# Kernel tuning notes

Measured on AMD Instinct MI355X. Metric: run time of the kernel, lower is better.

The kernel has to match this reference:

```python
import jax, jax.numpy as jnp
import numpy as np

B, T, C, NH = 8, 1024, 1024, 16
DH = C // NH  # 64


def setup_inputs() -> dict:
    key = jax.random.key(0)
    ks = jax.random.split(key, 7)
    s = 1.0 / np.sqrt(C)
    return {
        "x": jax.random.normal(ks[0], (B, T, C), dtype=jnp.float32),
        "Wq": jax.random.normal(ks[1], (C, C), dtype=jnp.float32) * s,
        "bq": jnp.zeros((C,), dtype=jnp.float32),
        "Wk": jax.random.normal(ks[2], (C, C), dtype=jnp.float32) * s,
        "bk": jnp.zeros((C,), dtype=jnp.float32),
        "Wv": jax.random.normal(ks[3], (C, C), dtype=jnp.float32) * s,
        "bv": jnp.zeros((C,), dtype=jnp.float32),
    }


def reference(x, Wq, bq, Wk, bk, Wv, bv):
    # Linear projections (weights stored as [in, out])
    q = x @ Wq + bq  # [B, T, C]
    k = x @ Wk + bk
    v = x @ Wv + bv
    q = q.reshape(B, T, NH, DH)
    k = k.reshape(B, T, NH, DH)
    v = v.reshape(B, T, NH, DH)
    scale = 1.0 / np.sqrt(DH)
    # NOTE: source module's causal mask buffer is all-ones due to a non-inplace
    # masked_fill bug, so attention is NON-causal (mask multiply is a no-op).
    attn = jnp.einsum("bqhd,bkhd->bhqk", q, k) * scale  # [B, NH, T, T]
    attn = jax.nn.softmax(attn, axis=-1)
    # dropout is identity (p=0 / eval)
    o = jnp.einsum("bhqk,bkhd->bqhd", attn, v)  # [B, T, NH, DH]
    return o.reshape(B, T, C)
```

## Files before the change

### kernel.cpp

```cpp
#include <hip/hip_runtime.h>


#define B_  8
#define T_  1024
#define C_  1024
#define NH_ 16
#define DH_ 64
#define M_  (B_ * T_)

typedef __bf16 bf16x8 __attribute__((ext_vector_type(8)));
typedef float  floatx4 __attribute__((ext_vector_type(4)));

__device__ __forceinline__ unsigned short f2bf(float f) {
    unsigned int u = __float_as_uint(f);
    unsigned int r = (u + 0x7fffu + ((u >> 16) & 1u)) >> 16;
    return (unsigned short)r;
}

__device__ __forceinline__ void gload_lds16(const void* g, void* l) {
    __builtin_amdgcn_global_load_lds(
        (const __attribute__((address_space(1))) unsigned int*)g,
        (__attribute__((address_space(3))) unsigned int*)l, 16, 0, 0);
}

__global__ __launch_bounds__(256) void cast_x_kernel(
    const float* __restrict__ x, unsigned short* __restrict__ xb, int n4)
{
    int i = blockIdx.x * 256 + threadIdx.x;
    if (i < n4) {
        float4 v = ((const float4*)x)[i];
        ushort4 o;
        o.x = f2bf(v.x); o.y = f2bf(v.y); o.z = f2bf(v.z); o.w = f2bf(v.w);
        ((ushort4*)xb)[i] = o;
    }
}

__global__ __launch_bounds__(256) void transpose_w_kernel(
    const float* __restrict__ Wq, const float* __restrict__ Wk,
    const float* __restrict__ Wv, unsigned short* __restrict__ WtAll)
{
    int which = blockIdx.y;
    const float* W = (which == 0) ? Wq : ((which == 1) ? Wk : Wv);
    unsigned short* out = WtAll + (size_t)which * C_ * C_;

    __shared__ __align__(16) unsigned short tile[64 * 65];
    int tb = blockIdx.x;
    int k0 = (tb >> 4) * 64, n0 = (tb & 15) * 64;
    int c = threadIdx.x & 63, r0 = threadIdx.x >> 6;

    for (int j = 0; j < 16; ++j) {
        int r = r0 + j * 4;
        tile[c * 65 + r] = f2bf(W[(size_t)(k0 + r) * C_ + n0 + c]);
    }
    __syncthreads();
    for (int j = 0; j < 16; ++j) {
        int r = r0 + j * 4;
        out[(size_t)(n0 + r) * C_ + k0 + c] = tile[r * 65 + c];
    }
}

__global__ __launch_bounds__(256) void qkv_gemm_kernel(
    const unsigned short* __restrict__ xb,
    const unsigned short* __restrict__ WtAll,
    const float* __restrict__ bq, const float* __restrict__ bk,
    const float* __restrict__ bv,
    unsigned short* __restrict__ Qb, unsigned short* __restrict__ Kb,
    unsigned short* __restrict__ Vb)
{
    int which = blockIdx.z;
    const unsigned short* W = WtAll + (size_t)which * C_ * C_;
    const float* bias = (which == 0) ? bq : ((which == 1) ? bk : bv);
    unsigned short* outp = (which == 0) ? Qb : ((which == 1) ? Kb : Vb);
    float oscale = (which == 0) ? 0.125f : 1.0f;

    __shared__ __align__(16) unsigned short As[128 * 64];
    __shared__ __align__(16) unsigned short Bs[128 * 64];

    int tid = threadIdx.x;
    int wave = tid >> 6, lane = tid & 63;
    int quad = lane >> 4, l16 = lane & 15, l7 = l16 & 7;
    int wm = wave >> 1, wn = wave & 1;
    int bm = blockIdx.x, bn = blockIdx.y;

    floatx4 acc[4][4] = {};

    for (int kk = 0; kk < C_; kk += 64) {
        __syncthreads();
        #pragma unroll
        for (int i = 0; i < 4; ++i) {
            int c = (wave * 4 + i) * 64 + lane;
            int row = c >> 3;
            int lcol = ((c & 7) ^ (row & 7)) * 8;
            gload_lds16(&xb[(size_t)(bm * 128 + row) * C_ + kk + lcol],
                        &As[(wave * 4 + i) * 512]);
            gload_lds16(&W[(size_t)(bn * 128 + row) * C_ + kk + lcol],
                        &Bs[(wave * 4 + i) * 512]);
        }
        __syncthreads();
        #pragma unroll
        for (int s = 0; s < 2; ++s) {
            bf16x8 a[4], bfr[4];
            #pragma unroll
            for (int mt = 0; mt < 4; ++mt) {
                int row = wm * 64 + mt * 16 + l16;
                a[mt] = *(const bf16x8*)&As[row * 64 + (((s * 4 + quad)) ^ l7) * 8];
            }
            #pragma unroll
            for (int nt = 0; nt < 4; ++nt) {
                int row = wn * 64 + nt * 16 + l16;
                bfr[nt] = *(const bf16x8*)&Bs[row * 64 + (((s * 4 + quad)) ^ l7) * 8];
            }
            #pragma unroll
            for (int mt = 0; mt < 4; ++mt)
                #pragma unroll
                for (int nt = 0; nt < 4; ++nt)
                    acc[mt][nt] = __builtin_amdgcn_mfma_f32_16x16x32_bf16(
                        a[mt], bfr[nt], acc[mt][nt], 0, 0, 0);
        }
    }

    #pragma unroll
    for (int nt = 0; nt < 4; ++nt) {
        int colg = bn * 128 + wn * 64 + nt * 16 + l16;
        int h = colg >> 6, d = colg & 63;
        float bval = bias[colg];
        #pragma unroll
        for (int mt = 0; mt < 4; ++mt) {
            #pragma unroll
            for (int reg = 0; reg < 4; ++reg) {
                int rowg = bm * 128 + wm * 64 + mt * 16 + quad * 4 + reg;
                int bb = rowg >> 10, t = rowg & (T_ - 1);
                float val = (acc[mt][nt][reg] + bval) * oscale;
                outp[((size_t)(bb * NH_ + h) * T_ + t) * DH_ + d] = f2bf(val);
            }
        }
    }
}

__global__ __launch_bounds__(256) void transpose_v_kernel(
    const unsigned short* __restrict__ Vb, unsigned short* __restrict__ Vt)
{
    int bh = blockIdx.y;
    int t0 = blockIdx.x * 64;
    const unsigned short* src = Vb + (size_t)bh * T_ * DH_;
    unsigned short* dst = Vt + (size_t)bh * DH_ * T_;
    __shared__ unsigned short tile[64 * 66];
    int c = threadIdx.x & 63, r0 = threadIdx.x >> 6;
    #pragma unroll
    for (int j = 0; j < 16; ++j) {
        int r = r0 * 16 + j;
        tile[r * 66 + c] = src[(size_t)(t0 + r) * DH_ + c];
    }
    __syncthreads();
    #pragma unroll
    for (int j = 0; j < 16; ++j) {
        int d = r0 * 16 + j;
        dst[(size_t)d * T_ + t0 + c] = tile[c * 66 + d];
    }
}

__global__ __launch_bounds__(256) void attn_kernel(
    const unsigned short* __restrict__ Qb,
    const unsigned short* __restrict__ Kb,
    const unsigned short* __restrict__ Vt,
    float* __restrict__ out)
{
    int bh = blockIdx.x;
    int qblk = blockIdx.y;
    int b = bh >> 4, h = bh & (NH_ - 1);
    int tid = threadIdx.x;
    int wave = tid >> 6, lane = tid & 63;
    int quad = lane >> 4, l16 = lane & 15, l7 = l16 & 7;

    const unsigned short* Qh = Qb + (size_t)bh * T_ * DH_;
    const unsigned short* Kh = Kb + (size_t)bh * T_ * DH_;
    const unsigned short* Vh = Vt + (size_t)bh * DH_ * T_;

    __shared__ __align__(16) unsigned short Ks[64 * 64];
    __shared__ __align__(16) unsigned short Vs[64 * 64];
    __shared__ __align__(16) unsigned short Ps[4][16 * 72];

    bf16x8 qa[2][2];
    #pragma unroll
    for (int mt = 0; mt < 2; ++mt) {
        int qrow = qblk * 128 + (wave * 2 + mt) * 16 + l16;
        qa[mt][0] = *(const bf16x8*)&Qh[(size_t)qrow * DH_ + quad * 8];
        qa[mt][1] = *(const bf16x8*)&Qh[(size_t)qrow * DH_ + 32 + quad * 8];
    }

    floatx4 o_acc[2][4] = {};
    float l_i[2][4] = {};

    for (int kt = 0; kt < T_ / 64; ++kt) {
        __syncthreads();
        #pragma unroll
        for (int i = 0; i < 2; ++i) {
            int c = (wave * 2 + i) * 64 + lane;
            int row = c >> 3;
            int lcol = ((c & 7) ^ (row & 7)) * 8;
            gload_lds16(&Kh[(size_t)(kt * 64 + row) * DH_ + lcol],
                        &Ks[(wave * 2 + i) * 512]);
            gload_lds16(&Vh[(size_t)row * T_ + kt * 64 + lcol],
                        &Vs[(wave * 2 + i) * 512]);
        }
        __syncthreads();

        bf16x8 kb[4][2];
        #pragma unroll
        for (int nt = 0; nt < 4; ++nt) {
            int r = (nt * 16 + l16) * 64;
            kb[nt][0] = *(const bf16x8*)&Ks[r + ((quad    ) ^ l7) * 8];
            kb[nt][1] = *(const bf16x8*)&Ks[r + ((quad + 4) ^ l7) * 8];
        }

        #pragma unroll
        for (int mt = 0; mt < 2; ++mt) {
            floatx4 s[4] = {};
            #pragma unroll
            for (int nt = 0; nt < 4; ++nt) {
                s[nt] = __builtin_amdgcn_mfma_f32_16x16x32_bf16(qa[mt][0], kb[nt][0], s[nt], 0, 0, 0);
                s[nt] = __builtin_amdgcn_mfma_f32_16x16x32_bf16(qa[mt][1], kb[nt][1], s[nt], 0, 0, 0);
            }
            #pragma unroll
            for (int reg = 0; reg < 4; ++reg) {
                float e0 = __expf(s[0][reg]), e1 = __expf(s[1][reg]);
                float e2 = __expf(s[2][reg]), e3 = __expf(s[3][reg]);
                s[0][reg] = e0; s[1][reg] = e1; s[2][reg] = e2; s[3][reg] = e3;
                float rs = (e0 + e1) + (e2 + e3);
                rs += __shfl_xor(rs, 1); rs += __shfl_xor(rs, 2);
                rs += __shfl_xor(rs, 4); rs += __shfl_xor(rs, 8);
                l_i[mt][reg] += rs;
            }
            #pragma unroll
            for (int nt = 0; nt < 4; ++nt)
                #pragma unroll
                for (int reg = 0; reg < 4; ++reg)
                    Ps[wave][(quad * 4 + reg) * 72 + nt * 16 + l16] = f2bf(s[nt][reg]);
            #pragma unroll
            for (int s2 = 0; s2 < 2; ++s2) {
                bf16x8 pa = *(const bf16x8*)&Ps[wave][l16 * 72 + s2 * 32 + quad * 8];
                #pragma unroll
                for (int nt = 0; nt < 4; ++nt) {
                    bf16x8 vb = *(const bf16x8*)&Vs[(nt * 16 + l16) * 64 + ((s2 * 4 + quad) ^ l7) * 8];
                    o_acc[mt][nt] = __builtin_amdgcn_mfma_f32_16x16x32_bf16(pa, vb, o_acc[mt][nt], 0, 0, 0);
                }
            }
        }
    }

    #pragma unroll
    for (int mt = 0; mt < 2; ++mt) {
        float inv[4];
        #pragma unroll
        for (int reg = 0; reg < 4; ++reg) inv[reg] = 1.0f / l_i[mt][reg];
        #pragma unroll
        for (int nt = 0; nt < 4; ++nt) {
            int d = nt * 16 + l16;
            #pragma unroll
            for (int reg = 0; reg < 4; ++reg) {
                int t = qblk * 128 + (wave * 2 + mt) * 16 + quad * 4 + reg;
                out[((size_t)b * T_ + t) * C_ + h * DH_ + d] = o_acc[mt][nt][reg] * inv[reg];
            }
        }
    }
}

extern "C" void kernel_launch(void* const* d_in, const int* in_sizes, int n_in,
                              void* d_out, int out_size, void* d_ws, size_t ws_size,
                              hipStream_t stream) {
    const float* x  = (const float*)d_in[0];
    const float* Wq = (const float*)d_in[1];
    const float* bq = (const float*)d_in[2];
    const float* Wk = (const float*)d_in[3];
    const float* bk = (const float*)d_in[4];
    const float* Wv = (const float*)d_in[5];
    const float* bv = (const float*)d_in[6];
    float* out = (float*)d_out;

    char* ws = (char*)d_ws;
    size_t off = 0;
    unsigned short* xb = (unsigned short*)(ws + off); off += (size_t)M_ * C_ * 2;
    unsigned short* Wt = (unsigned short*)(ws + off); off += (size_t)3 * C_ * C_ * 2;
    unsigned short* Qb = (unsigned short*)(ws + off); off += (size_t)M_ * C_ * 2;
    unsigned short* Kb = (unsigned short*)(ws + off); off += (size_t)M_ * C_ * 2;
    unsigned short* Vb = (unsigned short*)(ws + off); off += (size_t)M_ * C_ * 2;
    unsigned short* Vt = xb;

    int n4 = (M_ * C_) / 4;
    cast_x_kernel<<<dim3(n4 / 256), dim3(256), 0, stream>>>(x, xb, n4);

    transpose_w_kernel<<<dim3(256, 3), dim3(256), 0, stream>>>(Wq, Wk, Wv, Wt);

    qkv_gemm_kernel<<<dim3(M_ / 128, C_ / 128, 3), dim3(256), 0, stream>>>(
        xb, Wt, bq, bk, bv, Qb, Kb, Vb);

    transpose_v_kernel<<<dim3(T_ / 64, B_ * NH_), dim3(256), 0, stream>>>(Vb, Vt);

    attn_kernel<<<dim3(B_ * NH_, T_ / 128), dim3(256), 0, stream>>>(Qb, Kb, Vt, out);
}
```

Before: 250.7 us.

## Fuse V transpose into QKV epilogue and transpose attention MFMA operands

The QKV GEMM now writes V directly in transposed [bh, d, t] layout, which removes the separate transpose_v kernel launch and its extra read and write of V. The attention kernel swaps MFMA operand order so S^T and O^T are computed. That turns row sums into cross-quad shuffles, lets P be stored with vectorized ushort4 writes, and lets the output be stored as float4 rows. Softmax uses exp2f with log2e folded into the Q scale. The transposed V store in the GEMM epilogue is strided along t, so those writes are less coalesced.

```diff
diff --git a/kernel.cpp b/kernel.cpp
--- a/kernel.cpp
+++ b/kernel.cpp
@@ -65,13 +65,13 @@
     const float* __restrict__ bq, const float* __restrict__ bk,
     const float* __restrict__ bv,
     unsigned short* __restrict__ Qb, unsigned short* __restrict__ Kb,
-    unsigned short* __restrict__ Vb)
+    unsigned short* __restrict__ Vt)
 {
     int which = blockIdx.z;
     const unsigned short* W = WtAll + (size_t)which * C_ * C_;
     const float* bias = (which == 0) ? bq : ((which == 1) ? bk : bv);
-    unsigned short* outp = (which == 0) ? Qb : ((which == 1) ? Kb : Vb);
-    float oscale = (which == 0) ? 0.125f : 1.0f;
+    unsigned short* outp = (which == 0) ? Qb : ((which == 1) ? Kb : Vt);
+    float oscale = (which == 0) ? 0.125f * 1.44269504f : 1.0f;
 
     __shared__ __align__(16) unsigned short As[128 * 64];
     __shared__ __align__(16) unsigned short Bs[128 * 64];
@@ -131,31 +131,14 @@
                 int rowg = bm * 128 + wm * 64 + mt * 16 + quad * 4 + reg;
                 int bb = rowg >> 10, t = rowg & (T_ - 1);
                 float val = (acc[mt][nt][reg] + bval) * oscale;
-                outp[((size_t)(bb * NH_ + h) * T_ + t) * DH_ + d] = f2bf(val);
-            }
-        }
-    }
-}
-
-__global__ __launch_bounds__(256) void transpose_v_kernel(
-    const unsigned short* __restrict__ Vb, unsigned short* __restrict__ Vt)
-{
-    int bh = blockIdx.y;
-    int t0 = blockIdx.x * 64;
-    const unsigned short* src = Vb + (size_t)bh * T_ * DH_;
-    unsigned short* dst = Vt + (size_t)bh * DH_ * T_;
-    __shared__ unsigned short tile[64 * 66];
-    int c = threadIdx.x & 63, r0 = threadIdx.x >> 6;
-    #pragma unroll
-    for (int j = 0; j < 16; ++j) {
-        int r = r0 * 16 + j;
-        tile[r * 66 + c] = src[(size_t)(t0 + r) * DH_ + c];
-    }
-    __syncthreads();
-    #pragma unroll
-    for (int j = 0; j < 16; ++j) {
-        int d = r0 * 16 + j;
-        dst[(size_t)d * T_ + t0 + c] = tile[c * 66 + d];
+                size_t idx;
+                if (which < 2)
+                    idx = ((size_t)(bb * NH_ + h) * T_ + t) * DH_ + d;
+                else
+                    idx = ((size_t)(bb * NH_ + h) * DH_ + d) * T_ + t;
+                outp[idx] = f2bf(val);
+            }
+        }
     }
 }
 
@@ -178,7 +161,7 @@
 
     __shared__ __align__(16) unsigned short Ks[64 * 64];
     __shared__ __align__(16) unsigned short Vs[64 * 64];
-    __shared__ __align__(16) unsigned short Ps[4][16 * 72];
+    __shared__ __align__(16) unsigned short Ps[4][2][16 * 72];
 
     bf16x8 qa[2][2];
     #pragma unroll
@@ -189,7 +172,7 @@
     }
 
     floatx4 o_acc[2][4] = {};
-    float l_i[2][4] = {};
+    float l_i[2] = {0.0f, 0.0f};
 
     for (int kt = 0; kt < T_ / 64; ++kt) {
         __syncthreads();
@@ -205,62 +188,68 @@
         }
         __syncthreads();
 
-        bf16x8 kb[4][2];
+        floatx4 st[2][4] = {};
         #pragma unroll
         for (int nt = 0; nt < 4; ++nt) {
             int r = (nt * 16 + l16) * 64;
-            kb[nt][0] = *(const bf16x8*)&Ks[r + ((quad    ) ^ l7) * 8];
-            kb[nt][1] = *(const bf16x8*)&Ks[r + ((quad + 4) ^ l7) * 8];
+            bf16x8 k0 = *(const bf16x8*)&Ks[r + ((quad    ) ^ l7) * 8];
+            bf16x8 k1 = *(const bf16x8*)&Ks[r + ((quad + 4) ^ l7) * 8];
+            #pragma unroll
+            for (int mt = 0; mt < 2; ++mt) {
+                st[mt][nt] = __builtin_amdgcn_mfma_f32_16x16x32_bf16(k0, qa[mt][0], st[mt][nt], 0, 0, 0);
+                st[mt][nt] = __builtin_amdgcn_mfma_f32_16x16x32_bf16(k1, qa[mt][1], st[mt][nt], 0, 0, 0);
+            }
         }
 
         #pragma unroll
         for (int mt = 0; mt < 2; ++mt) {
-            floatx4 s[4] = {};
+            float rs = 0.0f;
             #pragma unroll
             for (int nt = 0; nt < 4; ++nt) {
-                s[nt] = __builtin_amdgcn_mfma_f32_16x16x32_bf16(qa[mt][0], kb[nt][0], s[nt], 0, 0, 0);
-                s[nt] = __builtin_amdgcn_mfma_f32_16x16x32_bf16(qa[mt][1], kb[nt][1], s[nt], 0, 0, 0);
-            }
-            #pragma unroll
-            for (int reg = 0; reg < 4; ++reg) {
-                float e0 = __expf(s[0][reg]), e1 = __expf(s[1][reg]);
-                float e2 = __expf(s[2][reg]), e3 = __expf(s[3][reg]);
-                s[0][reg] = e0; s[1][reg] = e1; s[2][reg] = e2; s[3][reg] = e3;
-                float rs = (e0 + e1) + (e2 + e3);
-                rs += __shfl_xor(rs, 1); rs += __shfl_xor(rs, 2);
-                rs += __shfl_xor(rs, 4); rs += __shfl_xor(rs, 8);
-                l_i[mt][reg] += rs;
-            }
-            #pragma unroll
-            for (int nt = 0; nt < 4; ++nt)
+                float e0 = exp2f(st[mt][nt][0]);
+                float e1 = exp2f(st[mt][nt][1]);
+                float e2 = exp2f(st[mt][nt][2]);
+                float e3 = exp2f(st[mt][nt][3]);
+                rs += (e0 + e1) + (e2 + e3);
+                ushort4 pk;
+                pk.x = f2bf(e0); pk.y = f2bf(e1); pk.z = f2bf(e2); pk.w = f2bf(e3);
+                *(ushort4*)&Ps[wave][mt][l16 * 72 + nt * 16 + quad * 4] = pk;
+            }
+            rs += __shfl_xor(rs, 16);
+            rs += __shfl_xor(rs, 32);
+            l_i[mt] += rs;
+        }
+
+        #pragma unroll
+        for (int s2 = 0; s2 < 2; ++s2) {
+            bf16x8 vb[4];
+            #pragma unroll
+            for (int dt = 0; dt < 4; ++dt)
+                vb[dt] = *(const bf16x8*)&Vs[(dt * 16 + l16) * 64 + ((s2 * 4 + quad) ^ l7) * 8];
+            #pragma unroll
+            for (int mt = 0; mt < 2; ++mt) {
+                bf16x8 pb = *(const bf16x8*)&Ps[wave][mt][l16 * 72 + s2 * 32 + quad * 8];
                 #pragma unroll
-                for (int reg = 0; reg < 4; ++reg)
-                    Ps[wave][(quad * 4 + reg) * 72 + nt * 16 + l16] = f2bf(s[nt][reg]);
-            #pragma unroll
-            for (int s2 = 0; s2 < 2; ++s2) {
-                bf16x8 pa = *(const bf16x8*)&Ps[wave][l16 * 72 + s2 * 32 + quad * 8];
-                #pragma unroll
-                for (int nt = 0; nt < 4; ++nt) {
-                    bf16x8 vb = *(const bf16x8*)&Vs[(nt * 16 + l16) * 64 + ((s2 * 4 + quad) ^ l7) * 8];
-                    o_acc[mt][nt] = __builtin_amdgcn_mfma_f32_16x16x32_bf16(pa, vb, o_acc[mt][nt], 0, 0, 0);
-                }
+                for (int dt = 0; dt < 4; ++dt)
+                    o_acc[mt][dt] = __builtin_amdgcn_mfma_f32_16x16x32_bf16(
+                        vb[dt], pb, o_acc[mt][dt], 0, 0, 0);
             }
         }
     }
 
     #pragma unroll
     for (int mt = 0; mt < 2; ++mt) {
-        float inv[4];
-        #pragma unroll
-        for (int reg = 0; reg < 4; ++reg) inv[reg] = 1.0f / l_i[mt][reg];
-        #pragma unroll
-        for (int nt = 0; nt < 4; ++nt) {
-            int d = nt * 16 + l16;
-            #pragma unroll
-            for (int reg = 0; reg < 4; ++reg) {
-                int t = qblk * 128 + (wave * 2 + mt) * 16 + quad * 4 + reg;
-                out[((size_t)b * T_ + t) * C_ + h * DH_ + d] = o_acc[mt][nt][reg] * inv[reg];
-            }
+        float inv = 1.0f / l_i[mt];
+        int t = qblk * 128 + (wave * 2 + mt) * 16 + l16;
+        float* op = &out[((size_t)b * T_ + t) * C_ + h * DH_];
+        #pragma unroll
+        for (int dt = 0; dt < 4; ++dt) {
+            float4 v;
+            v.x = o_acc[mt][dt][0] * inv;
+            v.y = o_acc[mt][dt][1] * inv;
+            v.z = o_acc[mt][dt][2] * inv;
+            v.w = o_acc[mt][dt][3] * inv;
+            *(float4*)&op[dt * 16 + quad * 4] = v;
         }
     }
 }
@@ -283,8 +272,7 @@
     unsigned short* Wt = (unsigned short*)(ws + off); off += (size_t)3 * C_ * C_ * 2;
     unsigned short* Qb = (unsigned short*)(ws + off); off += (size_t)M_ * C_ * 2;
     unsigned short* Kb = (unsigned short*)(ws + off); off += (size_t)M_ * C_ * 2;
-    unsigned short* Vb = (unsigned short*)(ws + off); off += (size_t)M_ * C_ * 2;
-    unsigned short* Vt = xb;
+    unsigned short* Vt = (unsigned short*)(ws + off); off += (size_t)M_ * C_ * 2;
 
     int n4 = (M_ * C_) / 4;
     cast_x_kernel<<<dim3(n4 / 256), dim3(256), 0, stream>>>(x, xb, n4);
@@ -292,9 +280,7 @@
     transpose_w_kernel<<<dim3(256, 3), dim3(256), 0, stream>>>(Wq, Wk, Wv, Wt);
 
     qkv_gemm_kernel<<<dim3(M_ / 128, C_ / 128, 3), dim3(256), 0, stream>>>(
-        xb, Wt, bq, bk, bv, Qb, Kb, Vb);
-
-    transpose_v_kernel<<<dim3(T_ / 64, B_ * NH_), dim3(256), 0, stream>>>(Vb, Vt);
+        xb, Wt, bq, bk, bv, Qb, Kb, Vt);
 
     attn_kernel<<<dim3(B_ * NH_, T_ / 128), dim3(256), 0, stream>>>(Qb, Kb, Vt, out);
 }
```

New measurement: 244.9 us. -2.3%, faster.
